# Kernel optimization log

Hardware: AMD Instinct MI355X
Metric: run time of the kernel (lower is better)

Reference implementation:

```python
import jax, jax.numpy as jnp
import numpy as np

M_BIT = 8      # BfpConfig.bfp_M_Bit: mantissa bits (incl. sign magnitude range)
GROUP = 16     # BFP block size along the reduction (last) dimension


def bfp_quant(x, m_bit=M_BIT, group=GROUP):
    """Block floating point quantize-dequantize along last dim.
    Each block of `group` values shares one exponent (exponent of block max);
    mantissas are rounded to (m_bit-1) magnitude bits + sign."""
    shape = x.shape
    xg = x.reshape(shape[:-1] + (shape[-1] // group, group))
    max_abs = jnp.max(jnp.abs(xg), axis=-1, keepdims=True)
    # shared exponent per block
    exp = jnp.floor(jnp.log2(jnp.maximum(max_abs, jnp.float32(1e-38))))
    scale = jnp.exp2(exp - (m_bit - 1))
    qmax = jnp.float32(2.0 ** (m_bit - 1) - 1.0)
    q = jnp.clip(jnp.round(xg / scale), -qmax, qmax) * scale
    q = jnp.where(max_abs > 0, q, jnp.zeros_like(q))
    return q.reshape(shape)


def setup_inputs() -> dict:
    key = jax.random.key(0)
    k1, k2, k3 = jax.random.split(key, 3)
    B, S, K, N = 8, 2048, 4096, 4096
    inp = jax.random.normal(k1, (B, S, K), dtype=jnp.float32)
    weight = jax.random.normal(k2, (N, K), dtype=jnp.float32) * 0.02
    bias = jax.random.normal(k3, (N,), dtype=jnp.float32) * 0.01
    return {"input": inp, "weight": weight, "bias": bias}


def reference(input, weight, bias):
    # BFP-quantize both GEMM operands along the shared reduction dim (K),
    # then dense GEMM + bias, matching BfpLinear.apply's forward.
    qx = bfp_quant(input)
    qw = bfp_quant(weight)
    out = jnp.einsum('bsk,nk->bsn', qx, qw)  # [B, S, N]
    return out + bias
```

## Files before the change

kernel.cpp:

```cpp
#include <hip/hip_runtime.h>
#include <cmath>

typedef __bf16 bf16;
typedef __bf16 bf16x4_t __attribute__((ext_vector_type(4)));
typedef __bf16 bf16x8_t __attribute__((ext_vector_type(8)));
typedef float f32x4 __attribute__((ext_vector_type(4)));

#define GAS __attribute__((address_space(1)))
#define LAS __attribute__((address_space(3)))

__global__ __launch_bounds__(256) void bfp_quant_f32_to_bf16(
    const float* __restrict__ x, bf16* __restrict__ y, long long n4) {
  long long t = (long long)blockIdx.x * 256 + threadIdx.x;
  if (t >= n4) return;
  const float4 v = reinterpret_cast<const float4*>(x)[t];

  float a = fmaxf(fmaxf(fabsf(v.x), fabsf(v.y)), fmaxf(fabsf(v.z), fabsf(v.w)));
  a = fmaxf(a, __shfl_xor(a, 1));
  a = fmaxf(a, __shfl_xor(a, 2));

  float q0, q1, q2, q3;
  if (a > 0.0f) {
    int ex = (int)((__float_as_uint(a) >> 23) & 0xffu) - 127;
    float scale = ldexpf(1.0f, ex - 7);
    float inv   = ldexpf(1.0f, 7 - ex);
    q0 = fminf(fmaxf(rintf(v.x * inv), -127.0f), 127.0f) * scale;
    q1 = fminf(fmaxf(rintf(v.y * inv), -127.0f), 127.0f) * scale;
    q2 = fminf(fmaxf(rintf(v.z * inv), -127.0f), 127.0f) * scale;
    q3 = fminf(fmaxf(rintf(v.w * inv), -127.0f), 127.0f) * scale;
  } else {
    q0 = q1 = q2 = q3 = 0.0f;
  }
  bf16x4_t o = { (__bf16)q0, (__bf16)q1, (__bf16)q2, (__bf16)q3 };
  reinterpret_cast<bf16x4_t*>(y)[t] = o;
}

#define BM 256
#define BN 256
#define BK 64
#define THREADS 512

#define PHASE_SYNC() do {                                   \
    asm volatile("" ::: "memory");                          \
    __builtin_amdgcn_s_barrier();                           \
    asm volatile("s_waitcnt lgkmcnt(0)" ::: "memory");      \
    __builtin_amdgcn_sched_barrier(0);                      \
  } while (0)

#define END_BAR() do {                                      \
    asm volatile("" ::: "memory");                          \
    __builtin_amdgcn_s_barrier();                           \
    asm volatile("" ::: "memory");                          \
  } while (0)

template <int H>
__device__ __forceinline__ void stage_half(const char* gb, char* ldsb,
                                           const int goff[4], long long kb,
                                           int tid) {
#pragma unroll
  for (int i = 2 * H; i < 2 * H + 2; ++i) {
    __builtin_amdgcn_global_load_lds(
        (const GAS unsigned int*)(gb + (goff[i] + kb)),
        (LAS unsigned int*)(ldsb + tid * 16 + i * 8192), 16, 0, 0);
  }
}

__global__ __launch_bounds__(THREADS, 2) void gemm_bf16_bt_8ph(
    const bf16* __restrict__ A,
    const bf16* __restrict__ B,
    const float* __restrict__ bias,
    float* __restrict__ C,
    int N, int K) {
  extern __shared__ char smem[];

  const int tid  = threadIdx.x;
  const int wave = tid >> 6;
  const int lane = tid & 63;
  const int wr   = wave >> 2;
  const int wc   = wave & 3;
  const int quad = lane >> 4;
  const int ln   = lane & 15;
  const int NT   = K / BK;

  const int gx   = gridDim.x;
  const int nwg  = gx * gridDim.y;
  const int orig = blockIdx.y * gx + blockIdx.x;
  const int swz  = (orig & 7) * (nwg >> 3) + (orig >> 3);
  const int bm   = swz / gx;
  const int bn   = swz % gx;

  const long long kstride = (long long)K * 2;
  const char* Ab = (const char*)A + (long long)bm * BM * kstride;
  const char* Bb = (const char*)B + (long long)bn * BN * kstride;

  int goff[4];
#pragma unroll
  for (int i = 0; i < 4; ++i) {
    const int o = tid * 16 + i * 8192;
    const int s = o >> 10;
    int w = o & 1023;
    w ^= ((w >> 9) & 1) << 5;
    const int grow = (s >> 1) * 16 + (w >> 6);
    const int gcb  = (s & 1) * 64 + (w & 63);
    goff[i] = grow * (K * 2) + gcb;
  }
  const int wofs = (ln * 64 + quad * 16) ^ ((ln & 8) << 2);

  char* const As0 = smem;
  char* const Bs0 = smem + 32768;
  char* const As1 = smem + 65536;
  char* const Bs1 = smem + 98304;

  f32x4 acc[8][4];
#pragma unroll
  for (int m = 0; m < 8; ++m)
#pragma unroll
    for (int n = 0; n < 4; ++n)
      acc[m][n] = (f32x4){0.0f, 0.0f, 0.0f, 0.0f};

  stage_half<0>(Ab, As0, goff, 0, tid);
  stage_half<1>(Ab, As0, goff, 0, tid);
  stage_half<0>(Bb, Bs0, goff, 0, tid);
  stage_half<1>(Bb, Bs0, goff, 0, tid);
  {
    const long long k1 = (NT > 1) ? (long long)BK * 2 : 0;
    stage_half<0>(Ab, As1, goff, k1, tid);
    stage_half<1>(Ab, As1, goff, k1, tid);
  }
  asm volatile("s_waitcnt vmcnt(4)" ::: "memory");
  __builtin_amdgcn_s_barrier();
  asm volatile("" ::: "memory");

  for (int t = 0; t < NT; ++t) {
    char* const Asc = (t & 1) ? As1 : As0;
    char* const Bsc = (t & 1) ? Bs1 : Bs0;
    char* const Bsn = (t & 1) ? Bs0 : Bs1;
    const long long kbB = (long long)((t + 1 < NT) ? t + 1 : NT - 1) * (BK * 2);
    const long long kbA = (long long)((t + 2 < NT) ? t + 2 : NT - 1) * (BK * 2);

    bf16x8_t a0[4][2], a1[4][2], b0[2][2], b1[2][2];

#pragma unroll
    for (int m = 0; m < 4; ++m)
#pragma unroll
      for (int ks = 0; ks < 2; ++ks)
        a0[m][ks] = *(const bf16x8_t*)(Asc + ((((wr * 8 + m) * 2 + ks) << 10) + wofs));
#pragma unroll
    for (int n = 0; n < 2; ++n)
#pragma unroll
      for (int ks = 0; ks < 2; ++ks)
        b0[n][ks] = *(const bf16x8_t*)(Bsc + ((((wc * 4 + n) * 2 + ks) << 10) + wofs));
    stage_half<0>(Bb, Bsn, goff, kbB, tid);
    PHASE_SYNC();
    __builtin_amdgcn_s_setprio(1);
#pragma unroll
    for (int m = 0; m < 4; ++m)
#pragma unroll
      for (int n = 0; n < 2; ++n)
#pragma unroll
        for (int ks = 0; ks < 2; ++ks)
          acc[m][n] = __builtin_amdgcn_mfma_f32_16x16x32_bf16(
              a0[m][ks], b0[n][ks], acc[m][n], 0, 0, 0);
    __builtin_amdgcn_s_setprio(0);
    END_BAR();

#pragma unroll
    for (int m = 0; m < 4; ++m)
#pragma unroll
      for (int ks = 0; ks < 2; ++ks)
        a1[m][ks] = *(const bf16x8_t*)(Asc + ((((wr * 8 + 4 + m) * 2 + ks) << 10) + wofs));
    stage_half<1>(Bb, Bsn, goff, kbB, tid);
    PHASE_SYNC();
    __builtin_amdgcn_s_setprio(1);
#pragma unroll
    for (int m = 0; m < 4; ++m)
#pragma unroll
      for (int n = 0; n < 2; ++n)
#pragma unroll
        for (int ks = 0; ks < 2; ++ks)
          acc[4 + m][n] = __builtin_amdgcn_mfma_f32_16x16x32_bf16(
              a1[m][ks], b0[n][ks], acc[4 + m][n], 0, 0, 0);
    __builtin_amdgcn_s_setprio(0);
    END_BAR();

#pragma unroll
    for (int n = 0; n < 2; ++n)
#pragma unroll
      for (int ks = 0; ks < 2; ++ks)
        b1[n][ks] = *(const bf16x8_t*)(Bsc + ((((wc * 4 + 2 + n) * 2 + ks) << 10) + wofs));
    stage_half<0>(Ab, Asc, goff, kbA, tid);
    PHASE_SYNC();
    __builtin_amdgcn_s_setprio(1);
#pragma unroll
    for (int m = 0; m < 4; ++m)
#pragma unroll
      for (int n = 0; n < 2; ++n)
#pragma unroll
        for (int ks = 0; ks < 2; ++ks)
          acc[4 + m][2 + n] = __builtin_amdgcn_mfma_f32_16x16x32_bf16(
              a1[m][ks], b1[n][ks], acc[4 + m][2 + n], 0, 0, 0);
    __builtin_amdgcn_s_setprio(0);
    END_BAR();

    stage_half<1>(Ab, Asc, goff, kbA, tid);
    PHASE_SYNC();
    __builtin_amdgcn_s_setprio(1);
#pragma unroll
    for (int m = 0; m < 4; ++m)
#pragma unroll
      for (int n = 0; n < 2; ++n)
#pragma unroll
        for (int ks = 0; ks < 2; ++ks)
          acc[m][2 + n] = __builtin_amdgcn_mfma_f32_16x16x32_bf16(
              a0[m][ks], b1[n][ks], acc[m][2 + n], 0, 0, 0);
    __builtin_amdgcn_s_setprio(0);
    asm volatile("s_waitcnt vmcnt(4)" ::: "memory");
    END_BAR();
  }
  asm volatile("s_waitcnt vmcnt(0)" ::: "memory");

  const long long row0 = (long long)bm * BM + wr * 128;
  const int col0 = bn * BN + wc * 64;
#pragma unroll
  for (int n = 0; n < 4; ++n) {
    const int col = col0 + n * 16 + ln;
    const float bv = bias[col];
#pragma unroll
    for (int m = 0; m < 8; ++m) {
      const long long row = row0 + m * 16 + quad * 4;
#pragma unroll
      for (int r = 0; r < 4; ++r)
        C[(row + r) * (long long)N + col] = acc[m][n][r] + bv;
    }
  }
}

extern "C" void kernel_launch(void* const* d_in, const int* in_sizes, int n_in,
                              void* d_out, int out_size, void* d_ws, size_t ws_size,
                              hipStream_t stream) {
  const float* inp    = (const float*)d_in[0];
  const float* weight = (const float*)d_in[1];
  const float* bias   = (const float*)d_in[2];
  float* out = (float*)d_out;

  const int N = in_sizes[2];
  const int K = in_sizes[1] / N;
  const int M = in_sizes[0] / K;

  const size_t qw_bytes  = (size_t)N * K * sizeof(bf16);
  const size_t row_bytes = (size_t)K * sizeof(bf16);

  long long Mc;
  if (ws_size >= qw_bytes + (size_t)M * row_bytes) {
    Mc = M;
  } else if (ws_size >= qw_bytes + (size_t)BM * row_bytes) {
    Mc = (long long)((ws_size - qw_bytes) / row_bytes) / BM * BM;
  } else {
    Mc = BM;
  }

  bf16* qw = (bf16*)d_ws;
  bf16* qx = (bf16*)((char*)d_ws + qw_bytes);

  static bool lds_attr_done = false;
  if (!lds_attr_done) {
    (void)hipFuncSetAttribute((const void*)gemm_bf16_bt_8ph,
                              hipFuncAttributeMaxDynamicSharedMemorySize,
                              131072);
    lds_attr_done = true;
  }

  const long long n4w = (long long)N * K / 4;
  hipLaunchKernelGGL(bfp_quant_f32_to_bf16, dim3((unsigned)((n4w + 255) / 256)),
                     dim3(256), 0, stream, weight, qw, n4w);

  for (long long m0 = 0; m0 < M; m0 += Mc) {
    const long long rows = (M - m0 < Mc) ? (M - m0) : Mc;
    const long long n4x  = rows * K / 4;
    hipLaunchKernelGGL(bfp_quant_f32_to_bf16, dim3((unsigned)((n4x + 255) / 256)),
                       dim3(256), 0, stream,
                       inp + m0 * K, qx, n4x);
    hipLaunchKernelGGL(gemm_bf16_bt_8ph,
                       dim3(N / BN, (unsigned)(rows / BM)), dim3(THREADS),
                       131072, stream,
                       qx, qw, bias, out + m0 * N, N, K);
  }
}
```

Before: 904.3 us.

## Software-pipeline LDS fragment loads across k-tiles and relax per-phase waits

Restructures the GEMM main loop so each k-tile's first A/B register fragments are read from LDS during the previous tile's last phase, and unrolls the loop by two with ping-pong register sets. The per-phase lgkmcnt(0) waits and sched barriers are removed, with only selective lgkmcnt/vmcnt waits kept. The aim is to hide LDS read latency behind MFMA work and cut barrier stalls, at the cost of more live registers and more delicate synchronisation that assumes an even tile count.

After: 1.211 ms. +33.9%, slower.

```diff
diff --git a/kernel.cpp b/kernel.cpp
--- a/kernel.cpp
+++ b/kernel.cpp
@@ -40,14 +40,7 @@
 #define BK 64
 #define THREADS 512
 
-#define PHASE_SYNC() do {                                   \
-    asm volatile("" ::: "memory");                          \
-    __builtin_amdgcn_s_barrier();                           \
-    asm volatile("s_waitcnt lgkmcnt(0)" ::: "memory");      \
-    __builtin_amdgcn_sched_barrier(0);                      \
-  } while (0)
-
-#define END_BAR() do {                                      \
+#define BAR() do {                                          \
     asm volatile("" ::: "memory");                          \
     __builtin_amdgcn_s_barrier();                           \
     asm volatile("" ::: "memory");                          \
@@ -63,6 +56,94 @@
         (const GAS unsigned int*)(gb + (goff[i] + kb)),
         (LAS unsigned int*)(ldsb + tid * 16 + i * 8192), 16, 0, 0);
   }
+}
+
+__device__ __forceinline__ void ktile(
+    char* const Asc, char* const Bsc, char* const Bsn, char* const AsN,
+    bf16x8_t (&a0)[4][2], bf16x8_t (&b0)[2][2],
+    bf16x8_t (&a0n)[4][2], bf16x8_t (&b0n)[2][2],
+    f32x4 (&acc)[8][4],
+    const char* Ab, const char* Bb, const int* goff,
+    long long kbB, long long kbA, int tid, int wofs, int wr, int wc) {
+  bf16x8_t a1[4][2], b1[2][2];
+
+#pragma unroll
+  for (int m = 0; m < 4; ++m)
+#pragma unroll
+    for (int ks = 0; ks < 2; ++ks)
+      a1[m][ks] = *(const bf16x8_t*)(Asc + ((((wr * 8 + 4 + m) * 2 + ks) << 10) + wofs));
+  stage_half<0>(Bb, Bsn, goff, kbB, tid);
+  BAR();
+  __builtin_amdgcn_s_setprio(1);
+#pragma unroll
+  for (int m = 0; m < 4; ++m)
+#pragma unroll
+    for (int n = 0; n < 2; ++n)
+#pragma unroll
+      for (int ks = 0; ks < 2; ++ks)
+        acc[m][n] = __builtin_amdgcn_mfma_f32_16x16x32_bf16(
+            a0[m][ks], b0[n][ks], acc[m][n], 0, 0, 0);
+  __builtin_amdgcn_s_setprio(0);
+  BAR();
+
+#pragma unroll
+  for (int n = 0; n < 2; ++n)
+#pragma unroll
+    for (int ks = 0; ks < 2; ++ks)
+      b1[n][ks] = *(const bf16x8_t*)(Bsc + ((((wc * 4 + 2 + n) * 2 + ks) << 10) + wofs));
+  stage_half<1>(Bb, Bsn, goff, kbB, tid);
+  BAR();
+  __builtin_amdgcn_s_setprio(1);
+#pragma unroll
+  for (int m = 0; m < 4; ++m)
+#pragma unroll
+    for (int n = 0; n < 2; ++n)
+#pragma unroll
+      for (int ks = 0; ks < 2; ++ks)
+        acc[4 + m][n] = __builtin_amdgcn_mfma_f32_16x16x32_bf16(
+            a1[m][ks], b0[n][ks], acc[4 + m][n], 0, 0, 0);
+  __builtin_amdgcn_s_setprio(0);
+  asm volatile("s_waitcnt lgkmcnt(0)" ::: "memory");
+  BAR();
+
+  stage_half<0>(Ab, Asc, goff, kbA, tid);
+  BAR();
+  __builtin_amdgcn_s_setprio(1);
+#pragma unroll
+  for (int m = 0; m < 4; ++m)
+#pragma unroll
+    for (int n = 0; n < 2; ++n)
+#pragma unroll
+      for (int ks = 0; ks < 2; ++ks)
+        acc[4 + m][2 + n] = __builtin_amdgcn_mfma_f32_16x16x32_bf16(
+            a1[m][ks], b1[n][ks], acc[4 + m][2 + n], 0, 0, 0);
+  __builtin_amdgcn_s_setprio(0);
+  asm volatile("s_waitcnt vmcnt(2)" ::: "memory");
+  BAR();
+
+#pragma unroll
+  for (int m = 0; m < 4; ++m)
+#pragma unroll
+    for (int ks = 0; ks < 2; ++ks)
+      a0n[m][ks] = *(const bf16x8_t*)(AsN + ((((wr * 8 + m) * 2 + ks) << 10) + wofs));
+#pragma unroll
+  for (int n = 0; n < 2; ++n)
+#pragma unroll
+    for (int ks = 0; ks < 2; ++ks)
+      b0n[n][ks] = *(const bf16x8_t*)(Bsn + ((((wc * 4 + n) * 2 + ks) << 10) + wofs));
+  stage_half<1>(Ab, Asc, goff, kbA, tid);
+  BAR();
+  __builtin_amdgcn_s_setprio(1);
+#pragma unroll
+  for (int m = 0; m < 4; ++m)
+#pragma unroll
+    for (int n = 0; n < 2; ++n)
+#pragma unroll
+      for (int ks = 0; ks < 2; ++ks)
+        acc[m][2 + n] = __builtin_amdgcn_mfma_f32_16x16x32_bf16(
+            a0[m][ks], b1[n][ks], acc[m][2 + n], 0, 0, 0);
+  __builtin_amdgcn_s_setprio(0);
+  BAR();
 }
 
 __global__ __launch_bounds__(THREADS, 2) void gemm_bf16_bt_8ph(
@@ -131,93 +212,29 @@
   __builtin_amdgcn_s_barrier();
   asm volatile("" ::: "memory");
 
-  for (int t = 0; t < NT; ++t) {
-    char* const Asc = (t & 1) ? As1 : As0;
-    char* const Bsc = (t & 1) ? Bs1 : Bs0;
-    char* const Bsn = (t & 1) ? Bs0 : Bs1;
-    const long long kbB = (long long)((t + 1 < NT) ? t + 1 : NT - 1) * (BK * 2);
-    const long long kbA = (long long)((t + 2 < NT) ? t + 2 : NT - 1) * (BK * 2);
-
-    bf16x8_t a0[4][2], a1[4][2], b0[2][2], b1[2][2];
-
-#pragma unroll
-    for (int m = 0; m < 4; ++m)
-#pragma unroll
-      for (int ks = 0; ks < 2; ++ks)
-        a0[m][ks] = *(const bf16x8_t*)(Asc + ((((wr * 8 + m) * 2 + ks) << 10) + wofs));
-#pragma unroll
-    for (int n = 0; n < 2; ++n)
-#pragma unroll
-      for (int ks = 0; ks < 2; ++ks)
-        b0[n][ks] = *(const bf16x8_t*)(Bsc + ((((wc * 4 + n) * 2 + ks) << 10) + wofs));
-    stage_half<0>(Bb, Bsn, goff, kbB, tid);
-    PHASE_SYNC();
-    __builtin_amdgcn_s_setprio(1);
-#pragma unroll
-    for (int m = 0; m < 4; ++m)
-#pragma unroll
-      for (int n = 0; n < 2; ++n)
-#pragma unroll
-        for (int ks = 0; ks < 2; ++ks)
-          acc[m][n] = __builtin_amdgcn_mfma_f32_16x16x32_bf16(
-              a0[m][ks], b0[n][ks], acc[m][n], 0, 0, 0);
-    __builtin_amdgcn_s_setprio(0);
-    END_BAR();
-
-#pragma unroll
-    for (int m = 0; m < 4; ++m)
-#pragma unroll
-      for (int ks = 0; ks < 2; ++ks)
-        a1[m][ks] = *(const bf16x8_t*)(Asc + ((((wr * 8 + 4 + m) * 2 + ks) << 10) + wofs));
-    stage_half<1>(Bb, Bsn, goff, kbB, tid);
-    PHASE_SYNC();
-    __builtin_amdgcn_s_setprio(1);
-#pragma unroll
-    for (int m = 0; m < 4; ++m)
-#pragma unroll
-      for (int n = 0; n < 2; ++n)
-#pragma unroll
-        for (int ks = 0; ks < 2; ++ks)
-          acc[4 + m][n] = __builtin_amdgcn_mfma_f32_16x16x32_bf16(
-              a1[m][ks], b0[n][ks], acc[4 + m][n], 0, 0, 0);
-    __builtin_amdgcn_s_setprio(0);
-    END_BAR();
-
-#pragma unroll
-    for (int n = 0; n < 2; ++n)
-#pragma unroll
-      for (int ks = 0; ks < 2; ++ks)
-        b1[n][ks] = *(const bf16x8_t*)(Bsc + ((((wc * 4 + 2 + n) * 2 + ks) << 10) + wofs));
-    stage_half<0>(Ab, Asc, goff, kbA, tid);
-    PHASE_SYNC();
-    __builtin_amdgcn_s_setprio(1);
-#pragma unroll
-    for (int m = 0; m < 4; ++m)
-#pragma unroll
-      for (int n = 0; n < 2; ++n)
-#pragma unroll
-        for (int ks = 0; ks < 2; ++ks)
-          acc[4 + m][2 + n] = __builtin_amdgcn_mfma_f32_16x16x32_bf16(
-              a1[m][ks], b1[n][ks], acc[4 + m][2 + n], 0, 0, 0);
-    __builtin_amdgcn_s_setprio(0);
-    END_BAR();
-
-    stage_half<1>(Ab, Asc, goff, kbA, tid);
-    PHASE_SYNC();
-    __builtin_amdgcn_s_setprio(1);
-#pragma unroll
-    for (int m = 0; m < 4; ++m)
-#pragma unroll
-      for (int n = 0; n < 2; ++n)
-#pragma unroll
-        for (int ks = 0; ks < 2; ++ks)
-          acc[m][2 + n] = __builtin_amdgcn_mfma_f32_16x16x32_bf16(
-              a0[m][ks], b1[n][ks], acc[m][2 + n], 0, 0, 0);
-    __builtin_amdgcn_s_setprio(0);
-    asm volatile("s_waitcnt vmcnt(4)" ::: "memory");
-    END_BAR();
-  }
-  asm volatile("s_waitcnt vmcnt(0)" ::: "memory");
+  bf16x8_t a0e[4][2], b0e[2][2], a0o[4][2], b0o[2][2];
+#pragma unroll
+  for (int m = 0; m < 4; ++m)
+#pragma unroll
+    for (int ks = 0; ks < 2; ++ks)
+      a0e[m][ks] = *(const bf16x8_t*)(As0 + ((((wr * 8 + m) * 2 + ks) << 10) + wofs));
+#pragma unroll
+  for (int n = 0; n < 2; ++n)
+#pragma unroll
+    for (int ks = 0; ks < 2; ++ks)
+      b0e[n][ks] = *(const bf16x8_t*)(Bs0 + ((((wc * 4 + n) * 2 + ks) << 10) + wofs));
+
+  for (int t = 0; t < NT; t += 2) {
+    const long long kbB0 = (long long)((t + 1 < NT) ? t + 1 : NT - 1) * (BK * 2);
+    const long long kbA0 = (long long)((t + 2 < NT) ? t + 2 : NT - 1) * (BK * 2);
+    const long long kbB1 = kbA0;
+    const long long kbA1 = (long long)((t + 3 < NT) ? t + 3 : NT - 1) * (BK * 2);
+    ktile(As0, Bs0, Bs1, As1, a0e, b0e, a0o, b0o, acc,
+          Ab, Bb, goff, kbB0, kbA0, tid, wofs, wr, wc);
+    ktile(As1, Bs1, Bs0, As0, a0o, b0o, a0e, b0e, acc,
+          Ab, Bb, goff, kbB1, kbA1, tid, wofs, wr, wc);
+  }
+  asm volatile("s_waitcnt vmcnt(0) lgkmcnt(0)" ::: "memory");
 
   const long long row0 = (long long)bm * BM + wr * 128;
   const int col0 = bn * BN + wc * 64;
```
